# Performance work log

Hardware: AMD Instinct MI355X
Metric: run time of the kernel (lower is better)

Reference implementation:

```python
import jax, jax.numpy as jnp
import numpy as np

B, N, C, A, H, W = 2, 5, 64, 2, 128, 256
COMM_THRESH = 0.01  # args['communication']['threshold']
SEL_TOPK = 2        # args['selector']['topk']


def _grid_sample(src, theta, Ho, Wo, mode):
    """torch affine_grid + grid_sample (align_corners=True, zero padding).
    src: (L,C,Hs,Ws), theta: (L,2,3) normalized affine, out: (L,C,Ho,Wo)."""
    L, Cc, Hs, Ws = src.shape
    xs = jnp.linspace(-1.0, 1.0, Wo, dtype=src.dtype)
    ys = jnp.linspace(-1.0, 1.0, Ho, dtype=src.dtype)
    gx, gy = jnp.meshgrid(xs, ys)                      # (Ho,Wo)
    base = jnp.stack([gx, gy, jnp.ones_like(gx)], -1)  # (Ho,Wo,3)
    coords = jnp.einsum('lij,hwj->lhwi', theta, base)  # (L,Ho,Wo,2)
    ix = (coords[..., 0] + 1.0) * 0.5 * (Ws - 1)
    iy = (coords[..., 1] + 1.0) * 0.5 * (Hs - 1)
    flat = src.reshape(L, Cc, Hs * Ws)

    def gather(yi, xi):
        valid = ((yi >= 0) & (yi < Hs) & (xi >= 0) & (xi < Ws)).astype(src.dtype)
        idx = jnp.clip(yi, 0, Hs - 1) * Ws + jnp.clip(xi, 0, Ws - 1)
        idx = jnp.broadcast_to(idx.reshape(L, 1, Ho * Wo), (L, Cc, Ho * Wo))
        v = jnp.take_along_axis(flat, idx, axis=2).reshape(L, Cc, Ho, Wo)
        return v * valid[:, None]

    if mode == 'nearest':
        return gather(jnp.round(iy).astype(jnp.int32), jnp.round(ix).astype(jnp.int32))
    x0 = jnp.floor(ix)
    y0 = jnp.floor(iy)
    wx = (ix - x0)[:, None]  # (L,1,Ho,Wo)
    wy = (iy - y0)[:, None]
    x0i = x0.astype(jnp.int32); y0i = y0.astype(jnp.int32)
    v00 = gather(y0i, x0i)
    v01 = gather(y0i, x0i + 1)
    v10 = gather(y0i + 1, x0i)
    v11 = gather(y0i + 1, x0i + 1)
    return (v00 * (1 - wy) * (1 - wx) + v01 * (1 - wy) * wx
            + v10 * wy * (1 - wx) + v11 * wy * wx)


def setup_inputs() -> dict:
    key = jax.random.key(0)
    k1, k2, k3 = jax.random.split(key, 3)
    x = jax.random.normal(k1, (B * N, C, H, W), jnp.float32)
    psm = jax.random.normal(k2, (B * N, A, H, W), jnp.float32)
    # near-identity affines: identity rotation + small random translation; diag = exact identity
    t = jax.random.uniform(k3, (B, N, N, 2), jnp.float32, -0.3, 0.3)
    t = t.at[:, jnp.arange(N), jnp.arange(N)].set(0.0)
    eye = jnp.tile(jnp.array([[1., 0., 0.], [0., 1., 0.]], jnp.float32), (B, N, N, 1, 1))
    nam = eye.at[..., 2].set(t)  # (B,N,N,2,3)
    return {"x": x, "psm_single": psm, "normalized_affine_matrix": nam, "record_len": N}


def reference(x, psm_single, normalized_affine_matrix, record_len):
    n = record_len
    sumN, c, h, w = x.shape
    b = normalized_affine_matrix.shape[0]
    # T_ego: row 0 of each batch's pairwise transform block, one (2,3) per agent
    theta = normalized_affine_matrix[:, 0].reshape(b * n, 2, 3).astype(x.dtype)
    vis = _grid_sample(jnp.ones((sumN, 1, h, w), x.dtype), theta, h, w, 'nearest')
    conf_w = _grid_sample(psm_single.astype(x.dtype), theta, h, w, 'bilinear')
    feats_w = _grid_sample(x, theta, h, w, 'bilinear')
    # communication masks: sigmoid confidence, max over anchors, threshold; ego always 1
    comm_map = jax.nn.sigmoid(conf_w).max(axis=1, keepdims=True)  # (sumN,1,h,w)
    comm = (comm_map > COMM_THRESH).astype(x.dtype)
    comm = comm.reshape(b, n, 1, h, w).at[:, 0].set(1.0).reshape(sumN, 1, h, w)
    # selector: top-k nearest non-ego agents by translation distance (hard, eval mode)
    t = normalized_affine_matrix[:, 0, :, :2, 2]                  # (b,n,2)
    dist2 = jnp.sum(t * t, axis=-1).at[:, 0].set(jnp.inf)        # exclude ego
    _, idx = jax.lax.top_k(-dist2, SEL_TOPK)                      # (b,k)
    owner = jnp.zeros((b, n), x.dtype).at[jnp.arange(b)[:, None], idx].set(1.0)
    owner = owner.at[:, 0].set(1.0)                               # max with ego mask
    final = comm * owner.reshape(sumN, 1, 1, 1)
    wx = feats_w * final
    num = (final * vis).reshape(sumN, -1).sum(-1)
    den = jnp.maximum(vis.reshape(sumN, -1).sum(-1), 1.0)
    effective_rate = (num / den).mean()
    x_out = wx.reshape(b, n, c, h, w).max(axis=1)                 # MaxFusion over agents
    return x_out, effective_rate
```

## Files before the change

kernel.cpp:

```cpp
#include <hip/hip_runtime.h>
#include <math.h>

namespace {
constexpr int Bc = 2, Nc = 5, Cc = 64, Ac = 2, Hc = 128, Wc = 256;
constexpr int SUMN = Bc * Nc;
constexpr int HW = Hc * Wc;
constexpr float LOGIT_THRESH = -4.59511985013459f;
constexpr int MASK_BLOCKS = (Bc * HW) / 256;
constexpr int FEAT_BLOCKS = (Bc * (Cc / 4) * Hc * (Wc / 4)) / 256;

constexpr int MASK_BYTE_OFF = 10240;

typedef float f4v __attribute__((ext_vector_type(4)));

__device__ __forceinline__ f4v load4u(const float* p) {
  f4v r;
  __builtin_memcpy(&r, p, sizeof(r));
  return r;
}

__device__ __forceinline__ unsigned owner_bits(const float* __restrict__ nam, int b) {
  float d2[Nc];
#pragma unroll
  for (int j = 0; j < Nc; ++j) {
    float tx = nam[(size_t)(b * Nc * Nc + j) * 6 + 2];
    float ty = nam[(size_t)(b * Nc * Nc + j) * 6 + 5];
    d2[j] = tx * tx + ty * ty;
  }
  d2[0] = INFINITY;
  int i1 = 1; float b1 = INFINITY;
#pragma unroll
  for (int j = 0; j < Nc; ++j) if (d2[j] < b1) { b1 = d2[j]; i1 = j; }
  int i2 = 1; float b2 = INFINITY;
#pragma unroll
  for (int j = 0; j < Nc; ++j) if (j != i1 && d2[j] < b2) { b2 = d2[j]; i2 = j; }
  return 1u | (1u << i1) | (1u << i2);
}

__global__ void __launch_bounds__(256) k_mask(const float* __restrict__ psm,
                                              const float* __restrict__ nam,
                                              int* __restrict__ partial,
                                              unsigned char* __restrict__ mask) {
  __shared__ int cnt[Nc * 2];
  int tid = threadIdx.x;
  if (tid < Nc * 2) cnt[tid] = 0;
  __syncthreads();

  int t = blockIdx.x * 256 + tid;
  int b = __builtin_amdgcn_readfirstlane(t >> 15);
  int h = (t >> 8) & (Hc - 1);
  int w = t & (Wc - 1);
  unsigned own = owner_bits(nam, b);
  float gx = -1.0f + (float)w * (2.0f / (Wc - 1));
  float gy = -1.0f + (float)h * (2.0f / (Hc - 1));
  unsigned m = 0;
#pragma unroll
  for (int j = 0; j < Nc; ++j) {
    int l = b * Nc + j;
    const float* th = nam + (size_t)(b * Nc * Nc + j) * 6;
    float cx = th[0] * gx + th[1] * gy + th[2];
    float cy = th[3] * gx + th[4] * gy + th[5];
    float ix = (cx + 1.0f) * 0.5f * (float)(Wc - 1);
    float iy = (cy + 1.0f) * 0.5f * (float)(Hc - 1);
    int rx = (int)rintf(ix), ry = (int)rintf(iy);
    int vis = (rx >= 0 && rx < Wc && ry >= 0 && ry < Hc) ? 1 : 0;
    int comm = 1;
    if (j != 0) {
      float x0f = floorf(ix), y0f = floorf(iy);
      float fx = ix - x0f, fy = iy - y0f;
      int x0 = (int)x0f, y0 = (int)y0f;
      int x1 = x0 + 1, y1 = y0 + 1;
      bool vx0 = (x0 >= 0) && (x0 < Wc), vx1 = (x1 >= 0) && (x1 < Wc);
      bool vy0 = (y0 >= 0) && (y0 < Hc), vy1 = (y1 >= 0) && (y1 < Hc);
      int cx0 = min(max(x0, 0), Wc - 1), cx1 = min(max(x1, 0), Wc - 1);
      int cy0 = min(max(y0, 0), Hc - 1), cy1 = min(max(y1, 0), Hc - 1);
      int o00 = cy0 * Wc + cx0, o01 = cy0 * Wc + cx1;
      int o10 = cy1 * Wc + cx0, o11 = cy1 * Wc + cx1;
      float w00 = (vy0 && vx0) ? (1.0f - fy) * (1.0f - fx) : 0.0f;
      float w01 = (vy0 && vx1) ? (1.0f - fy) * fx : 0.0f;
      float w10 = (vy1 && vx0) ? fy * (1.0f - fx) : 0.0f;
      float w11 = (vy1 && vx1) ? fy * fx : 0.0f;
      float vmax = -INFINITY;
#pragma unroll
      for (int a = 0; a < Ac; ++a) {
        const float* p = psm + (size_t)(l * Ac + a) * HW;
        float v = p[o00] * w00 + p[o01] * w01 + p[o10] * w10 + p[o11] * w11;
        vmax = fmaxf(vmax, v);
      }
      comm = (vmax > LOGIT_THRESH) ? 1 : 0;
    }
    int fin = comm & (int)((own >> j) & 1u);
    m |= (unsigned)fin << j;
    unsigned long long bv = __ballot(vis != 0);
    unsigned long long bf = __ballot((fin & vis) != 0);
    if ((tid & 63) == 0) {
      atomicAdd(&cnt[j * 2 + 0], (int)__popcll(bv));
      atomicAdd(&cnt[j * 2 + 1], (int)__popcll(bf));
    }
  }
  mask[t] = (unsigned char)m;
  __syncthreads();
  if (tid < Nc * 2) partial[blockIdx.x * (Nc * 2) + tid] = cnt[tid];
}

__global__ void __launch_bounds__(256) k_feat(const float* __restrict__ x,
                                              const float* __restrict__ nam,
                                              const unsigned char* __restrict__ mask,
                                              const int* __restrict__ partial,
                                              float* __restrict__ out) {
  if (blockIdx.x == FEAT_BLOCKS) {
    int lane = threadIdx.x;
    if (lane < 64) {
      float s = 0.0f;
      for (int l = 0; l < SUMN; ++l) {
        int b = l / Nc, j = l % Nc;
        int vis = 0, num = 0;
#pragma unroll
        for (int k = 0; k < 2; ++k) {
          int blk = b * (MASK_BLOCKS / Bc) + lane + 64 * k;
          vis += partial[blk * (Nc * 2) + j * 2 + 0];
          num += partial[blk * (Nc * 2) + j * 2 + 1];
        }
#pragma unroll
        for (int off = 32; off; off >>= 1) {
          vis += __shfl_down(vis, off);
          num += __shfl_down(num, off);
        }
        if (lane == 0) s += (float)num / fmaxf((float)vis, 1.0f);
      }
      if (lane == 0) out[(size_t)Bc * Cc * HW] = s / (float)SUMN;
    }
    return;
  }

  int q = blockIdx.x * 256 + threadIdx.x;
  int w0 = (q & 63) << 2;
  int h = (q >> 6) & (Hc - 1);
  int c4 = (q >> 13) & (Cc / 4 - 1);
  int b = q >> 17;
  int bs = __builtin_amdgcn_readfirstlane(b);

  unsigned mm4;
  __builtin_memcpy(&mm4, mask + (size_t)bs * HW + h * Wc + w0, 4);

  float gy = -1.0f + (float)h * (2.0f / (Hc - 1));
  float best[4][4];
#pragma unroll
  for (int c = 0; c < 4; ++c)
#pragma unroll
    for (int k = 0; k < 4; ++k) best[c][k] = 0.0f;

#pragma unroll
  for (int j = 0; j < Nc; ++j) {
    if ((mm4 & (0x01010101u << j)) == 0) continue;
    int l = bs * Nc + j;
    const float* th = nam + (size_t)(bs * Nc * Nc + j) * 6;
    float t00 = th[0], t01 = th[1], t02 = th[2];
    float t10 = th[3], t11 = th[4], t12 = th[5];

    float ix[4], iy[4], fx[4], fy[4];
    int x0i[4], y0i[4];
#pragma unroll
    for (int k = 0; k < 4; ++k) {
      float gx = -1.0f + (float)(w0 + k) * (2.0f / (Wc - 1));
      float cx = t00 * gx + t01 * gy + t02;
      float cy = t10 * gx + t11 * gy + t12;
      ix[k] = (cx + 1.0f) * 0.5f * (float)(Wc - 1);
      iy[k] = (cy + 1.0f) * 0.5f * (float)(Hc - 1);
      float x0f = floorf(ix[k]), y0f = floorf(iy[k]);
      fx[k] = ix[k] - x0f; fy[k] = iy[k] - y0f;
      x0i[k] = (int)x0f; y0i[k] = (int)y0f;
    }
    int X0 = x0i[0], Y0 = y0i[0];
    bool fast = (x0i[1] == X0 + 1) && (x0i[2] == X0 + 2) && (x0i[3] == X0 + 3) &&
                (y0i[1] == Y0) && (y0i[2] == Y0) && (y0i[3] == Y0) &&
                (X0 >= 0) && (X0 + 4 < Wc);
    const float* xb = x + (size_t)(l * Cc + c4 * 4) * HW;

    if (fast) {
      bool vy0 = (Y0 >= 0) && (Y0 < Hc), vy1 = (Y0 + 1 >= 0) && (Y0 + 1 < Hc);
      int cy0 = min(max(Y0, 0), Hc - 1), cy1 = min(max(Y0 + 1, 0), Hc - 1);
      int r0off = cy0 * Wc + X0, r1off = cy1 * Wc + X0;
      float wy0[4], wy1[4];
#pragma unroll
      for (int k = 0; k < 4; ++k) {
        wy0[k] = vy0 ? (1.0f - fy[k]) : 0.0f;
        wy1[k] = vy1 ? fy[k] : 0.0f;
      }
      const float* p = xb;
#pragma unroll
      for (int c = 0; c < 4; ++c) {
        f4v a0 = load4u(p + r0off); float a0e = p[r0off + 4];
        f4v a1 = load4u(p + r1off); float a1e = p[r1off + 4];
        float r0[5] = {a0.x, a0.y, a0.z, a0.w, a0e};
        float r1[5] = {a1.x, a1.y, a1.z, a1.w, a1e};
#pragma unroll
        for (int k = 0; k < 4; ++k) {
          float val = wy0[k] * (r0[k] * (1.0f - fx[k]) + r0[k + 1] * fx[k]) +
                      wy1[k] * (r1[k] * (1.0f - fx[k]) + r1[k + 1] * fx[k]);
          val = ((mm4 >> (8 * k + j)) & 1u) ? val : 0.0f;
          best[c][k] = fmaxf(best[c][k], val);
        }
        p += HW;
      }
    } else {
#pragma unroll
      for (int k = 0; k < 4; ++k) {
        if (((mm4 >> (8 * k + j)) & 1u) == 0) continue;
        int x0 = x0i[k], y0 = y0i[k], x1 = x0 + 1, y1 = y0 + 1;
        bool vx0 = (x0 >= 0) && (x0 < Wc), vx1 = (x1 >= 0) && (x1 < Wc);
        bool vy0 = (y0 >= 0) && (y0 < Hc), vy1 = (y1 >= 0) && (y1 < Hc);
        int cx0 = min(max(x0, 0), Wc - 1), cx1 = min(max(x1, 0), Wc - 1);
        int cy0 = min(max(y0, 0), Hc - 1), cy1 = min(max(y1, 0), Hc - 1);
        int o00 = cy0 * Wc + cx0, o01 = cy0 * Wc + cx1;
        int o10 = cy1 * Wc + cx0, o11 = cy1 * Wc + cx1;
        float w00 = (vy0 && vx0) ? (1.0f - fy[k]) * (1.0f - fx[k]) : 0.0f;
        float w01 = (vy0 && vx1) ? (1.0f - fy[k]) * fx[k] : 0.0f;
        float w10 = (vy1 && vx0) ? fy[k] * (1.0f - fx[k]) : 0.0f;
        float w11 = (vy1 && vx1) ? fy[k] * fx[k] : 0.0f;
        const float* p = xb;
#pragma unroll
        for (int c = 0; c < 4; ++c) {
          float val = p[o00] * w00 + p[o01] * w01 + p[o10] * w10 + p[o11] * w11;
          best[c][k] = fmaxf(best[c][k], val);
          p += HW;
        }
      }
    }
  }

  size_t obase = (size_t)(bs * Cc + c4 * 4) * HW + h * Wc + w0;
#pragma unroll
  for (int c = 0; c < 4; ++c) {
    f4v v = {best[c][0], best[c][1], best[c][2], best[c][3]};
    __builtin_nontemporal_store(v, (f4v*)(out + obase + (size_t)c * HW));
  }
}

}

extern "C" void kernel_launch(void* const* d_in, const int* in_sizes, int n_in,
                              void* d_out, int out_size, void* d_ws, size_t ws_size,
                              hipStream_t stream) {
  const float* x = (const float*)d_in[0];
  const float* psm = (const float*)d_in[1];
  const float* nam = (const float*)d_in[2];
  float* out = (float*)d_out;
  int* partial = (int*)d_ws;
  unsigned char* mask = (unsigned char*)d_ws + MASK_BYTE_OFF;

  hipLaunchKernelGGL(k_mask, dim3(MASK_BLOCKS), dim3(256), 0, stream, psm, nam, partial, mask);
  hipLaunchKernelGGL(k_feat, dim3(FEAT_BLOCKS + 1), dim3(256), 0, stream, x, nam, mask, partial,
                     out);
}
```

Measured before the change: 139.6 us.

## Fuse mask and feature kernels into one cooperative persistent kernel with grid sync

Merges the mask-building and feature-fusion kernels into a single cooperative launch of 512 persistent blocks separated by a grid-wide barrier. This removes the second kernel launch and the gap between the two kernels. Each feature thread now covers 2 channels instead of 4 and loops 4 times. The trade-offs are the grid-sync cost, a persistent grid that may underfill the GPU, and less channel reuse per coordinate computation.

Result: slower. 262.7 us (+88.2%).

```diff
diff --git a/kernel.cpp b/kernel.cpp
--- a/kernel.cpp
+++ b/kernel.cpp
@@ -1,5 +1,8 @@
 #include <hip/hip_runtime.h>
+#include <hip/hip_cooperative_groups.h>
 #include <math.h>
+
+namespace cg = cooperative_groups;
 
 namespace {
 constexpr int Bc = 2, Nc = 5, Cc = 64, Ac = 2, Hc = 128, Wc = 256;
@@ -7,7 +10,8 @@
 constexpr int HW = Hc * Wc;
 constexpr float LOGIT_THRESH = -4.59511985013459f;
 constexpr int MASK_BLOCKS = (Bc * HW) / 256;
-constexpr int FEAT_BLOCKS = (Bc * (Cc / 4) * Hc * (Wc / 4)) / 256;
+constexpr int GRID = 512;
+constexpr int FEAT_ITERS = 4;
 
 constexpr int MASK_BYTE_OFF = 10240;
 
@@ -37,203 +41,205 @@
   return 1u | (1u << i1) | (1u << i2);
 }
 
-__global__ void __launch_bounds__(256) k_mask(const float* __restrict__ psm,
-                                              const float* __restrict__ nam,
-                                              int* __restrict__ partial,
-                                              unsigned char* __restrict__ mask) {
+__global__ void __launch_bounds__(256, 2) k_all(const float* __restrict__ x,
+                                                const float* __restrict__ psm,
+                                                const float* __restrict__ nam,
+                                                int* __restrict__ partial,
+                                                unsigned char* __restrict__ mask,
+                                                float* __restrict__ out) {
   __shared__ int cnt[Nc * 2];
   int tid = threadIdx.x;
-  if (tid < Nc * 2) cnt[tid] = 0;
-  __syncthreads();
-
-  int t = blockIdx.x * 256 + tid;
-  int b = __builtin_amdgcn_readfirstlane(t >> 15);
-  int h = (t >> 8) & (Hc - 1);
-  int w = t & (Wc - 1);
-  unsigned own = owner_bits(nam, b);
-  float gx = -1.0f + (float)w * (2.0f / (Wc - 1));
-  float gy = -1.0f + (float)h * (2.0f / (Hc - 1));
-  unsigned m = 0;
-#pragma unroll
-  for (int j = 0; j < Nc; ++j) {
-    int l = b * Nc + j;
-    const float* th = nam + (size_t)(b * Nc * Nc + j) * 6;
-    float cx = th[0] * gx + th[1] * gy + th[2];
-    float cy = th[3] * gx + th[4] * gy + th[5];
-    float ix = (cx + 1.0f) * 0.5f * (float)(Wc - 1);
-    float iy = (cy + 1.0f) * 0.5f * (float)(Hc - 1);
-    int rx = (int)rintf(ix), ry = (int)rintf(iy);
-    int vis = (rx >= 0 && rx < Wc && ry >= 0 && ry < Hc) ? 1 : 0;
-    int comm = 1;
-    if (j != 0) {
-      float x0f = floorf(ix), y0f = floorf(iy);
-      float fx = ix - x0f, fy = iy - y0f;
-      int x0 = (int)x0f, y0 = (int)y0f;
-      int x1 = x0 + 1, y1 = y0 + 1;
-      bool vx0 = (x0 >= 0) && (x0 < Wc), vx1 = (x1 >= 0) && (x1 < Wc);
-      bool vy0 = (y0 >= 0) && (y0 < Hc), vy1 = (y1 >= 0) && (y1 < Hc);
-      int cx0 = min(max(x0, 0), Wc - 1), cx1 = min(max(x1, 0), Wc - 1);
-      int cy0 = min(max(y0, 0), Hc - 1), cy1 = min(max(y1, 0), Hc - 1);
-      int o00 = cy0 * Wc + cx0, o01 = cy0 * Wc + cx1;
-      int o10 = cy1 * Wc + cx0, o11 = cy1 * Wc + cx1;
-      float w00 = (vy0 && vx0) ? (1.0f - fy) * (1.0f - fx) : 0.0f;
-      float w01 = (vy0 && vx1) ? (1.0f - fy) * fx : 0.0f;
-      float w10 = (vy1 && vx0) ? fy * (1.0f - fx) : 0.0f;
-      float w11 = (vy1 && vx1) ? fy * fx : 0.0f;
-      float vmax = -INFINITY;
-#pragma unroll
-      for (int a = 0; a < Ac; ++a) {
-        const float* p = psm + (size_t)(l * Ac + a) * HW;
-        float v = p[o00] * w00 + p[o01] * w01 + p[o10] * w10 + p[o11] * w11;
-        vmax = fmaxf(vmax, v);
-      }
-      comm = (vmax > LOGIT_THRESH) ? 1 : 0;
-    }
-    int fin = comm & (int)((own >> j) & 1u);
-    m |= (unsigned)fin << j;
-    unsigned long long bv = __ballot(vis != 0);
-    unsigned long long bf = __ballot((fin & vis) != 0);
-    if ((tid & 63) == 0) {
-      atomicAdd(&cnt[j * 2 + 0], (int)__popcll(bv));
-      atomicAdd(&cnt[j * 2 + 1], (int)__popcll(bf));
-    }
-  }
-  mask[t] = (unsigned char)m;
-  __syncthreads();
-  if (tid < Nc * 2) partial[blockIdx.x * (Nc * 2) + tid] = cnt[tid];
-}
-
-__global__ void __launch_bounds__(256) k_feat(const float* __restrict__ x,
-                                              const float* __restrict__ nam,
-                                              const unsigned char* __restrict__ mask,
-                                              const int* __restrict__ partial,
-                                              float* __restrict__ out) {
-  if (blockIdx.x == FEAT_BLOCKS) {
-    int lane = threadIdx.x;
-    if (lane < 64) {
-      float s = 0.0f;
-      for (int l = 0; l < SUMN; ++l) {
-        int b = l / Nc, j = l % Nc;
-        int vis = 0, num = 0;
-#pragma unroll
-        for (int k = 0; k < 2; ++k) {
-          int blk = b * (MASK_BLOCKS / Bc) + lane + 64 * k;
-          vis += partial[blk * (Nc * 2) + j * 2 + 0];
-          num += partial[blk * (Nc * 2) + j * 2 + 1];
-        }
-#pragma unroll
-        for (int off = 32; off; off >>= 1) {
-          vis += __shfl_down(vis, off);
-          num += __shfl_down(num, off);
-        }
-        if (lane == 0) s += (float)num / fmaxf((float)vis, 1.0f);
-      }
-      if (lane == 0) out[(size_t)Bc * Cc * HW] = s / (float)SUMN;
-    }
-    return;
-  }
-
-  int q = blockIdx.x * 256 + threadIdx.x;
-  int w0 = (q & 63) << 2;
-  int h = (q >> 6) & (Hc - 1);
-  int c4 = (q >> 13) & (Cc / 4 - 1);
-  int b = q >> 17;
-  int bs = __builtin_amdgcn_readfirstlane(b);
-
-  unsigned mm4;
-  __builtin_memcpy(&mm4, mask + (size_t)bs * HW + h * Wc + w0, 4);
-
-  float gy = -1.0f + (float)h * (2.0f / (Hc - 1));
-  float best[4][4];
-#pragma unroll
-  for (int c = 0; c < 4; ++c)
-#pragma unroll
-    for (int k = 0; k < 4; ++k) best[c][k] = 0.0f;
-
-#pragma unroll
-  for (int j = 0; j < Nc; ++j) {
-    if ((mm4 & (0x01010101u << j)) == 0) continue;
-    int l = bs * Nc + j;
-    const float* th = nam + (size_t)(bs * Nc * Nc + j) * 6;
-    float t00 = th[0], t01 = th[1], t02 = th[2];
-    float t10 = th[3], t11 = th[4], t12 = th[5];
-
-    float ix[4], iy[4], fx[4], fy[4];
-    int x0i[4], y0i[4];
-#pragma unroll
-    for (int k = 0; k < 4; ++k) {
-      float gx = -1.0f + (float)(w0 + k) * (2.0f / (Wc - 1));
-      float cx = t00 * gx + t01 * gy + t02;
-      float cy = t10 * gx + t11 * gy + t12;
-      ix[k] = (cx + 1.0f) * 0.5f * (float)(Wc - 1);
-      iy[k] = (cy + 1.0f) * 0.5f * (float)(Hc - 1);
-      float x0f = floorf(ix[k]), y0f = floorf(iy[k]);
-      fx[k] = ix[k] - x0f; fy[k] = iy[k] - y0f;
-      x0i[k] = (int)x0f; y0i[k] = (int)y0f;
-    }
-    int X0 = x0i[0], Y0 = y0i[0];
-    bool fast = (x0i[1] == X0 + 1) && (x0i[2] == X0 + 2) && (x0i[3] == X0 + 3) &&
-                (y0i[1] == Y0) && (y0i[2] == Y0) && (y0i[3] == Y0) &&
-                (X0 >= 0) && (X0 + 4 < Wc);
-    const float* xb = x + (size_t)(l * Cc + c4 * 4) * HW;
-
-    if (fast) {
-      bool vy0 = (Y0 >= 0) && (Y0 < Hc), vy1 = (Y0 + 1 >= 0) && (Y0 + 1 < Hc);
-      int cy0 = min(max(Y0, 0), Hc - 1), cy1 = min(max(Y0 + 1, 0), Hc - 1);
-      int r0off = cy0 * Wc + X0, r1off = cy1 * Wc + X0;
-      float wy0[4], wy1[4];
-#pragma unroll
-      for (int k = 0; k < 4; ++k) {
-        wy0[k] = vy0 ? (1.0f - fy[k]) : 0.0f;
-        wy1[k] = vy1 ? fy[k] : 0.0f;
-      }
-      const float* p = xb;
-#pragma unroll
-      for (int c = 0; c < 4; ++c) {
-        f4v a0 = load4u(p + r0off); float a0e = p[r0off + 4];
-        f4v a1 = load4u(p + r1off); float a1e = p[r1off + 4];
-        float r0[5] = {a0.x, a0.y, a0.z, a0.w, a0e};
-        float r1[5] = {a1.x, a1.y, a1.z, a1.w, a1e};
-#pragma unroll
-        for (int k = 0; k < 4; ++k) {
-          float val = wy0[k] * (r0[k] * (1.0f - fx[k]) + r0[k + 1] * fx[k]) +
-                      wy1[k] * (r1[k] * (1.0f - fx[k]) + r1[k + 1] * fx[k]);
-          val = ((mm4 >> (8 * k + j)) & 1u) ? val : 0.0f;
-          best[c][k] = fmaxf(best[c][k], val);
-        }
-        p += HW;
-      }
-    } else {
-#pragma unroll
-      for (int k = 0; k < 4; ++k) {
-        if (((mm4 >> (8 * k + j)) & 1u) == 0) continue;
-        int x0 = x0i[k], y0 = y0i[k], x1 = x0 + 1, y1 = y0 + 1;
+  int blk = blockIdx.x;
+
+  if (blk < MASK_BLOCKS) {
+    if (tid < Nc * 2) cnt[tid] = 0;
+    __syncthreads();
+
+    int t = blk * 256 + tid;
+    int b = __builtin_amdgcn_readfirstlane(t >> 15);
+    int h = (t >> 8) & (Hc - 1);
+    int w = t & (Wc - 1);
+    unsigned own = owner_bits(nam, b);
+    float gx = -1.0f + (float)w * (2.0f / (Wc - 1));
+    float gy = -1.0f + (float)h * (2.0f / (Hc - 1));
+    unsigned m = 0;
+#pragma unroll
+    for (int j = 0; j < Nc; ++j) {
+      int l = b * Nc + j;
+      const float* th = nam + (size_t)(b * Nc * Nc + j) * 6;
+      float cx = th[0] * gx + th[1] * gy + th[2];
+      float cy = th[3] * gx + th[4] * gy + th[5];
+      float ix = (cx + 1.0f) * 0.5f * (float)(Wc - 1);
+      float iy = (cy + 1.0f) * 0.5f * (float)(Hc - 1);
+      int rx = (int)rintf(ix), ry = (int)rintf(iy);
+      int vis = (rx >= 0 && rx < Wc && ry >= 0 && ry < Hc) ? 1 : 0;
+      int comm = 1;
+      if (j != 0) {
+        float x0f = floorf(ix), y0f = floorf(iy);
+        float fx = ix - x0f, fy = iy - y0f;
+        int x0 = (int)x0f, y0 = (int)y0f;
+        int x1 = x0 + 1, y1 = y0 + 1;
         bool vx0 = (x0 >= 0) && (x0 < Wc), vx1 = (x1 >= 0) && (x1 < Wc);
         bool vy0 = (y0 >= 0) && (y0 < Hc), vy1 = (y1 >= 0) && (y1 < Hc);
         int cx0 = min(max(x0, 0), Wc - 1), cx1 = min(max(x1, 0), Wc - 1);
         int cy0 = min(max(y0, 0), Hc - 1), cy1 = min(max(y1, 0), Hc - 1);
         int o00 = cy0 * Wc + cx0, o01 = cy0 * Wc + cx1;
         int o10 = cy1 * Wc + cx0, o11 = cy1 * Wc + cx1;
-        float w00 = (vy0 && vx0) ? (1.0f - fy[k]) * (1.0f - fx[k]) : 0.0f;
-        float w01 = (vy0 && vx1) ? (1.0f - fy[k]) * fx[k] : 0.0f;
-        float w10 = (vy1 && vx0) ? fy[k] * (1.0f - fx[k]) : 0.0f;
-        float w11 = (vy1 && vx1) ? fy[k] * fx[k] : 0.0f;
+        float w00 = (vy0 && vx0) ? (1.0f - fy) * (1.0f - fx) : 0.0f;
+        float w01 = (vy0 && vx1) ? (1.0f - fy) * fx : 0.0f;
+        float w10 = (vy1 && vx0) ? fy * (1.0f - fx) : 0.0f;
+        float w11 = (vy1 && vx1) ? fy * fx : 0.0f;
+        float vmax = -INFINITY;
+#pragma unroll
+        for (int a = 0; a < Ac; ++a) {
+          const float* p = psm + (size_t)(l * Ac + a) * HW;
+          float v = p[o00] * w00 + p[o01] * w01 + p[o10] * w10 + p[o11] * w11;
+          vmax = fmaxf(vmax, v);
+        }
+        comm = (vmax > LOGIT_THRESH) ? 1 : 0;
+      }
+      int fin = comm & (int)((own >> j) & 1u);
+      m |= (unsigned)fin << j;
+      unsigned long long bv = __ballot(vis != 0);
+      unsigned long long bf = __ballot((fin & vis) != 0);
+      if ((tid & 63) == 0) {
+        atomicAdd(&cnt[j * 2 + 0], (int)__popcll(bv));
+        atomicAdd(&cnt[j * 2 + 1], (int)__popcll(bf));
+      }
+    }
+    mask[t] = (unsigned char)m;
+    __syncthreads();
+    if (tid < Nc * 2) partial[blk * (Nc * 2) + tid] = cnt[tid];
+  }
+
+  __threadfence();
+  cg::this_grid().sync();
+
+  if (blk == 0 && tid < 64) {
+    int lane = tid;
+    float s = 0.0f;
+    for (int l = 0; l < SUMN; ++l) {
+      int b = l / Nc, j = l % Nc;
+      int vis = 0, num = 0;
+#pragma unroll
+      for (int k = 0; k < 2; ++k) {
+        int mblk = b * (MASK_BLOCKS / Bc) + lane + 64 * k;
+        vis += partial[mblk * (Nc * 2) + j * 2 + 0];
+        num += partial[mblk * (Nc * 2) + j * 2 + 1];
+      }
+#pragma unroll
+      for (int off = 32; off; off >>= 1) {
+        vis += __shfl_down(vis, off);
+        num += __shfl_down(num, off);
+      }
+      if (lane == 0) s += (float)num / fmaxf((float)vis, 1.0f);
+    }
+    if (lane == 0) out[(size_t)Bc * Cc * HW] = s / (float)SUMN;
+  }
+
+  for (int it = 0; it < FEAT_ITERS; ++it) {
+    int u = (it * GRID + blk) * 256 + tid;
+    int w0 = (u & 63) << 2;
+    int h = (u >> 6) & (Hc - 1);
+    int c = ((u >> 13) & (Cc / 2 - 1)) * 2;
+    int b = u >> 18;
+    int bs = __builtin_amdgcn_readfirstlane(b);
+
+    unsigned mm4;
+    __builtin_memcpy(&mm4, mask + (size_t)bs * HW + h * Wc + w0, 4);
+
+    float gy = -1.0f + (float)h * (2.0f / (Hc - 1));
+    float best[2][4];
+#pragma unroll
+    for (int cc = 0; cc < 2; ++cc)
+#pragma unroll
+      for (int k = 0; k < 4; ++k) best[cc][k] = 0.0f;
+
+#pragma unroll
+    for (int j = 0; j < Nc; ++j) {
+      if ((mm4 & (0x01010101u << j)) == 0) continue;
+      int l = bs * Nc + j;
+      const float* th = nam + (size_t)(bs * Nc * Nc + j) * 6;
+      float t00 = th[0], t01 = th[1], t02 = th[2];
+      float t10 = th[3], t11 = th[4], t12 = th[5];
+
+      float fx[4], fy[4];
+      int x0i[4], y0i[4];
+#pragma unroll
+      for (int k = 0; k < 4; ++k) {
+        float gx = -1.0f + (float)(w0 + k) * (2.0f / (Wc - 1));
+        float cx = t00 * gx + t01 * gy + t02;
+        float cy = t10 * gx + t11 * gy + t12;
+        float ix = (cx + 1.0f) * 0.5f * (float)(Wc - 1);
+        float iy = (cy + 1.0f) * 0.5f * (float)(Hc - 1);
+        float x0f = floorf(ix), y0f = floorf(iy);
+        fx[k] = ix - x0f; fy[k] = iy - y0f;
+        x0i[k] = (int)x0f; y0i[k] = (int)y0f;
+      }
+      int X0 = x0i[0], Y0 = y0i[0];
+      bool fast = (x0i[1] == X0 + 1) && (x0i[2] == X0 + 2) && (x0i[3] == X0 + 3) &&
+                  (y0i[1] == Y0) && (y0i[2] == Y0) && (y0i[3] == Y0) &&
+                  (X0 >= 0) && (X0 + 4 < Wc);
+      const float* xb = x + (size_t)(l * Cc + c) * HW;
+
+      if (fast) {
+        bool vy0 = (Y0 >= 0) && (Y0 < Hc), vy1 = (Y0 + 1 >= 0) && (Y0 + 1 < Hc);
+        int cy0 = min(max(Y0, 0), Hc - 1), cy1 = min(max(Y0 + 1, 0), Hc - 1);
+        int r0off = cy0 * Wc + X0, r1off = cy1 * Wc + X0;
+        float wy0[4], wy1[4];
+#pragma unroll
+        for (int k = 0; k < 4; ++k) {
+          wy0[k] = vy0 ? (1.0f - fy[k]) : 0.0f;
+          wy1[k] = vy1 ? fy[k] : 0.0f;
+        }
         const float* p = xb;
 #pragma unroll
-        for (int c = 0; c < 4; ++c) {
-          float val = p[o00] * w00 + p[o01] * w01 + p[o10] * w10 + p[o11] * w11;
-          best[c][k] = fmaxf(best[c][k], val);
+        for (int cc = 0; cc < 2; ++cc) {
+          f4v a0 = load4u(p + r0off); float a0e = p[r0off + 4];
+          f4v a1 = load4u(p + r1off); float a1e = p[r1off + 4];
+          float r0[5] = {a0.x, a0.y, a0.z, a0.w, a0e};
+          float r1[5] = {a1.x, a1.y, a1.z, a1.w, a1e};
+#pragma unroll
+          for (int k = 0; k < 4; ++k) {
+            float val = wy0[k] * (r0[k] * (1.0f - fx[k]) + r0[k + 1] * fx[k]) +
+                        wy1[k] * (r1[k] * (1.0f - fx[k]) + r1[k + 1] * fx[k]);
+            val = ((mm4 >> (8 * k + j)) & 1u) ? val : 0.0f;
+            best[cc][k] = fmaxf(best[cc][k], val);
+          }
           p += HW;
         }
-      }
-    }
-  }
-
-  size_t obase = (size_t)(bs * Cc + c4 * 4) * HW + h * Wc + w0;
-#pragma unroll
-  for (int c = 0; c < 4; ++c) {
-    f4v v = {best[c][0], best[c][1], best[c][2], best[c][3]};
-    __builtin_nontemporal_store(v, (f4v*)(out + obase + (size_t)c * HW));
+      } else {
+#pragma unroll
+        for (int k = 0; k < 4; ++k) {
+          if (((mm4 >> (8 * k + j)) & 1u) == 0) continue;
+          int x0 = x0i[k], y0 = y0i[k], x1 = x0 + 1, y1 = y0 + 1;
+          bool vx0 = (x0 >= 0) && (x0 < Wc), vx1 = (x1 >= 0) && (x1 < Wc);
+          bool vy0 = (y0 >= 0) && (y0 < Hc), vy1 = (y1 >= 0) && (y1 < Hc);
+          int cx0 = min(max(x0, 0), Wc - 1), cx1 = min(max(x1, 0), Wc - 1);
+          int cy0 = min(max(y0, 0), Hc - 1), cy1 = min(max(y1, 0), Hc - 1);
+          int o00 = cy0 * Wc + cx0, o01 = cy0 * Wc + cx1;
+          int o10 = cy1 * Wc + cx0, o11 = cy1 * Wc + cx1;
+          float w00 = (vy0 && vx0) ? (1.0f - fy[k]) * (1.0f - fx[k]) : 0.0f;
+          float w01 = (vy0 && vx1) ? (1.0f - fy[k]) * fx[k] : 0.0f;
+          float w10 = (vy1 && vx0) ? fy[k] * (1.0f - fx[k]) : 0.0f;
+          float w11 = (vy1 && vx1) ? fy[k] * fx[k] : 0.0f;
+          const float* p = xb;
+#pragma unroll
+          for (int cc = 0; cc < 2; ++cc) {
+            float val = p[o00] * w00 + p[o01] * w01 + p[o10] * w10 + p[o11] * w11;
+            best[cc][k] = fmaxf(best[cc][k], val);
+            p += HW;
+          }
+        }
+      }
+    }
+
+    size_t obase = (size_t)(bs * Cc + c) * HW + h * Wc + w0;
+#pragma unroll
+    for (int cc = 0; cc < 2; ++cc) {
+      f4v v = {best[cc][0], best[cc][1], best[cc][2], best[cc][3]};
+      __builtin_nontemporal_store(v, (f4v*)(out + obase + (size_t)cc * HW));
+    }
   }
 }
 
@@ -249,7 +255,7 @@
   int* partial = (int*)d_ws;
   unsigned char* mask = (unsigned char*)d_ws + MASK_BYTE_OFF;
 
-  hipLaunchKernelGGL(k_mask, dim3(MASK_BLOCKS), dim3(256), 0, stream, psm, nam, partial, mask);
-  hipLaunchKernelGGL(k_feat, dim3(FEAT_BLOCKS + 1), dim3(256), 0, stream, x, nam, mask, partial,
-                     out);
-}
+  void* args[] = {(void*)&x, (void*)&psm, (void*)&nam, (void*)&partial, (void*)&mask,
+                  (void*)&out};
+  hipLaunchCooperativeKernel((const void*)k_all, dim3(GRID), dim3(256), args, 0, stream);
+}
```
